# Performance work log

Hardware: AMD Instinct MI355X
Metric: run time of the kernel (lower is better)

The kernel has to match this reference:

```python
import jax, jax.numpy as jnp
import numpy as np

D_MODEL = 8      # group_channel_num = ceil(64/8)
D_INNER = 16     # expand*d_model
D_STATE = 16
D_CONV = 4
DT_RANK = 1      # ceil(d_model/16)
TOKEN_NUM = 8
GN_GROUPS = 4
EPS = 1e-5


def setup_inputs() -> dict:
    key = jax.random.key(0)
    ks = jax.random.split(key, 12)
    b, c, h, w = 4, 64, 128, 128
    s = 0.1
    return {
        "x": jax.random.normal(ks[0], (b, c, h, w), jnp.float32),
        "W_in": jax.random.normal(ks[1], (2 * D_INNER, D_MODEL), jnp.float32) * s,
        "w_conv": jax.random.normal(ks[2], (D_INNER, D_CONV), jnp.float32) * s,
        "b_conv": jax.random.normal(ks[3], (D_INNER,), jnp.float32) * s,
        "W_xproj": jax.random.normal(ks[4], (DT_RANK + 2 * D_STATE, D_INNER), jnp.float32) * s,
        "W_dt": jax.random.normal(ks[5], (D_INNER, DT_RANK), jnp.float32) * s,
        "b_dt": jax.random.normal(ks[6], (D_INNER,), jnp.float32) * s,
        "A_log": jnp.log(jnp.tile(jnp.arange(1, D_STATE + 1, dtype=jnp.float32), (D_INNER, 1))),
        "D": jnp.ones((D_INNER,), jnp.float32),
        "W_out": jax.random.normal(ks[7], (D_MODEL, D_INNER), jnp.float32) * s,
        "gamma": jnp.ones((c,), jnp.float32),
        "beta": jnp.zeros((c,), jnp.float32),
    }


def _mamba(xf, W_in, w_conv, b_conv, W_xproj, W_dt, b_dt, A_log, D, W_out):
    # xf: (N, L, d_model)
    N, L, _ = xf.shape
    xz = jnp.einsum("nld,ed->nle", xf, W_in)            # (N, L, 2*d_inner)
    xm, z = jnp.split(xz, 2, axis=-1)
    # depthwise causal conv1d, kernel d_conv, truncated to L
    xp = jnp.pad(xm, ((0, 0), (D_CONV - 1, 0), (0, 0)))
    xc = b_conv + sum(xp[:, k:k + L, :] * w_conv[:, k] for k in range(D_CONV))
    xc = jax.nn.silu(xc)                                  # (N, L, d_inner)
    dbl = jnp.einsum("nli,ei->nle", xc, W_xproj)
    dt = dbl[..., :DT_RANK]
    B = dbl[..., DT_RANK:DT_RANK + D_STATE]               # (N, L, d_state)
    C = dbl[..., DT_RANK + D_STATE:]                      # (N, L, d_state)
    delta = jax.nn.softplus(jnp.einsum("nlr,ir->nli", dt, W_dt) + b_dt)
    A = -jnp.exp(A_log)                                   # (d_inner, d_state)
    dA = jnp.exp(delta[..., None] * A)                    # (N, L, d_inner, d_state)
    dBu = delta[..., None] * B[:, :, None, :] * xc[..., None]

    def step(hst, inp):
        dA_t, dBu_t, C_t = inp
        hst = dA_t * hst + dBu_t                          # (N, d_inner, d_state)
        y_t = jnp.einsum("nis,ns->ni", hst, C_t)
        return hst, y_t

    h0 = jnp.zeros((N, D_INNER, D_STATE), xf.dtype)
    _, ys = jax.lax.scan(step, h0, (jnp.swapaxes(dA, 0, 1),
                                    jnp.swapaxes(dBu, 0, 1),
                                    jnp.swapaxes(C, 0, 1)))
    y = jnp.swapaxes(ys, 0, 1)                            # (N, L, d_inner)
    y = y + D * xc
    y = y * jax.nn.silu(z)
    return jnp.einsum("nli,oi->nlo", y, W_out)


def reference(x, W_in, w_conv, b_conv, W_xproj, W_dt, b_dt, A_log, D, W_out, gamma, beta):
    b, c, h, w = x.shape  # c == channel_num == 64, no padding needed
    xt = jnp.transpose(x, (0, 2, 3, 1)).reshape(b * h * w, TOKEN_NUM, D_MODEL)
    y = _mamba(xt, W_in, w_conv, b_conv, W_xproj, W_dt, b_dt, A_log, D, W_out)
    y = y.reshape(b, h, w, c)
    y = jnp.transpose(y, (0, 3, 1, 2))                    # (b, c, h, w)
    # GroupNorm(groups=4) + SiLU
    yr = y.reshape(b, GN_GROUPS, c // GN_GROUPS, h, w)
    mu = yr.mean(axis=(2, 3, 4), keepdims=True)
    var = yr.var(axis=(2, 3, 4), keepdims=True)
    yn = ((yr - mu) * jax.lax.rsqrt(var + EPS)).reshape(b, c, h, w)
    yn = yn * gamma[:, None, None] + beta[:, None, None]
    return x + jax.nn.silu(yn)
```

## Files before the change

kernel.cpp:

```cpp
#include <hip/hip_runtime.h>
#include <math.h>

#define BATCH 4
#define CCH 64
#define HW 16384
#define LL 8
#define DI 16
#define NSEQ (BATCH*HW)
#define CNT_PER_GROUP (16*HW)

__device__ __forceinline__ float siluf(float v) {
    return v * __builtin_amdgcn_rcpf(1.f + __expf(-v));
}

__global__ __launch_bounds__(256, 4) void mamba_kernel(
    const float* __restrict__ x, const float* __restrict__ W_in,
    const float* __restrict__ w_conv, const float* __restrict__ b_conv,
    const float* __restrict__ W_xproj, const float* __restrict__ W_dt,
    const float* __restrict__ b_dt, const float* __restrict__ Dp,
    const float* __restrict__ W_out,
    float* __restrict__ y_out,
    float* __restrict__ stats)
{
    __shared__ float xf_lds[16][68];
    __shared__ float xcy_lds[LL][16][20];
    __shared__ unsigned int proj_lds[LL][16][18];
    __shared__ float wx_lds[33][20];
    __shared__ float wout_lds[8][20];
    __shared__ float wsum_lds[4][8];

    const int t = threadIdx.x;
    const int n0 = blockIdx.x * 16;
    const int b = n0 / HW;
    const int p0 = n0 % HW;

    for (int j = t; j < 33 * 16; j += 256) wx_lds[j >> 4][j & 15] = W_xproj[j];
    for (int j = t; j < 8 * 16; j += 256) wout_lds[j >> 4][j & 15] = W_out[j];

    {
        const int wofs = t & 15;
        const int cbase = t >> 4;
        const float* xb = x + (size_t)b * CCH * HW + p0 + wofs;
#pragma unroll
        for (int it = 0; it < 4; ++it) {
            int c = cbase + 16 * it;
            xf_lds[wofs][c] = xb[(size_t)c * HW];
        }
    }

    const int s = t >> 4;
    const int i = t & 15;

    const float4 wm0 = *(const float4*)&W_in[i * 8];
    const float4 wm1 = *(const float4*)&W_in[i * 8 + 4];
    const float4 wz0 = *(const float4*)&W_in[(16 + i) * 8];
    const float4 wz1 = *(const float4*)&W_in[(16 + i) * 8 + 4];
    const float4 wcv = *(const float4*)&w_conv[i * 4];
    const float bc  = b_conv[i];
    const float wdt = W_dt[i];
    const float bdt = b_dt[i];
    const float Di  = Dp[i];

    __syncthreads();

    float xm[LL], zz[LL], xcv[LL];
#pragma unroll
    for (int l = 0; l < LL; ++l) {
        float4 xa = *(const float4*)&xf_lds[s][l * 8];
        float4 xb4 = *(const float4*)&xf_lds[s][l * 8 + 4];
        xm[l] = xa.x * wm0.x + xa.y * wm0.y + xa.z * wm0.z + xa.w * wm0.w
              + xb4.x * wm1.x + xb4.y * wm1.y + xb4.z * wm1.z + xb4.w * wm1.w;
        zz[l] = xa.x * wz0.x + xa.y * wz0.y + xa.z * wz0.z + xa.w * wz0.w
              + xb4.x * wz1.x + xb4.y * wz1.y + xb4.z * wz1.z + xb4.w * wz1.w;
    }
#pragma unroll
    for (int l = 0; l < LL; ++l) {
        float acc = bc + wcv.w * xm[l];
        if (l >= 1) acc += wcv.z * xm[l - 1];
        if (l >= 2) acc += wcv.y * xm[l - 2];
        if (l >= 3) acc += wcv.x * xm[l - 3];
        float sv = siluf(acc);
        xcv[l] = sv;
        xcy_lds[l][s][i] = sv;
    }

    float4 w0q[4], wBq[4], wCq[4];
#pragma unroll
    for (int k = 0; k < 4; ++k) {
        w0q[k] = *(const float4*)&wx_lds[0][k * 4];
        wBq[k] = *(const float4*)&wx_lds[1 + i][k * 4];
        wCq[k] = *(const float4*)&wx_lds[17 + i][k * 4];
    }
    __syncthreads();

    float dtv[LL];
#pragma unroll
    for (int l = 0; l < LL; ++l) {
        float aB = 0.f, aC = 0.f, a0 = 0.f;
#pragma unroll
        for (int k = 0; k < 4; ++k) {
            float4 xc = *(const float4*)&xcy_lds[l][s][k * 4];
            aB += xc.x * wBq[k].x + xc.y * wBq[k].y + xc.z * wBq[k].z + xc.w * wBq[k].w;
            aC += xc.x * wCq[k].x + xc.y * wCq[k].y + xc.z * wCq[k].z + xc.w * wCq[k].w;
            a0 += xc.x * w0q[k].x + xc.y * w0q[k].y + xc.z * w0q[k].z + xc.w * w0q[k].w;
        }
        unsigned int ub = (__float_as_uint(aB) + 0x8000u) >> 16;
        unsigned int uc = (__float_as_uint(aC) + 0x8000u) & 0xFFFF0000u;
        proj_lds[l][s][i] = ub | uc;
        dtv[l] = a0;
    }
    __syncthreads();

    float hst[16];
#pragma unroll
    for (int q = 0; q < 16; ++q) hst[q] = 0.f;
#pragma unroll
    for (int l = 0; l < LL; ++l) {
        float pre = dtv[l] * wdt + bdt;
        float e = __expf(pre);
        float r = __builtin_amdgcn_rcpf(1.f + e);
        float delta = (pre > 15.f) ? pre : -__logf(r);
        float u = xcv[l];
        float du = delta * u;

        unsigned int pk[16];
#pragma unroll
        for (int k = 0; k < 4; ++k)
            *(uint4*)&pk[k * 4] = *(const uint4*)&proj_lds[l][s][k * 4];

        float pw = 1.f, yl = 0.f;
#pragma unroll
        for (int q = 0; q < 16; ++q) {
            float Bv = __uint_as_float(pk[q] << 16);
            float Cv = __uint_as_float(pk[q] & 0xFFFF0000u);
            pw *= r;
            hst[q] = pw * hst[q] + du * Bv;
            yl += hst[q] * Cv;
        }
        yl += Di * u;
        yl *= siluf(zz[l]);
        xcy_lds[l][s][i] = yl;
    }
    __syncthreads();

    const int s4 = t & 15;
    const int c4 = t >> 4;
    float gsum[4], gsq[4];
#pragma unroll
    for (int it = 0; it < 4; ++it) {
        int c = c4 + 16 * it;
        int l = c >> 3, o = c & 7;
        float acc = 0.f;
#pragma unroll
        for (int k = 0; k < 4; ++k) {
            float4 yv = *(const float4*)&xcy_lds[l][s4][k * 4];
            float4 wo = *(const float4*)&wout_lds[o][k * 4];
            acc += yv.x * wo.x + yv.y * wo.y + yv.z * wo.z + yv.w * wo.w;
        }
        y_out[((size_t)b * CCH + c) * HW + p0 + s4] = acc;
        gsum[it] = acc; gsq[it] = acc * acc;
    }
#pragma unroll
    for (int ofs = 32; ofs > 0; ofs >>= 1) {
#pragma unroll
        for (int it = 0; it < 4; ++it) {
            gsum[it] += __shfl_down(gsum[it], ofs, 64);
            gsq[it]  += __shfl_down(gsq[it], ofs, 64);
        }
    }
    const int wave = t >> 6;
    if ((t & 63) == 0) {
#pragma unroll
        for (int it = 0; it < 4; ++it) {
            wsum_lds[wave][it * 2]     = gsum[it];
            wsum_lds[wave][it * 2 + 1] = gsq[it];
        }
    }
    __syncthreads();
    if (t < 8) {
        float v = wsum_lds[0][t] + wsum_lds[1][t] + wsum_lds[2][t] + wsum_lds[3][t];
        int g = t >> 1, which = t & 1;
        atomicAdd(&stats[(b * 4 + g) * 2 + which], v);
    }
}

__global__ __launch_bounds__(256) void gn_kernel(
    const float* __restrict__ x, const float* __restrict__ gamma,
    const float* __restrict__ beta, const float* __restrict__ stats,
    float* __restrict__ y)
{
    const float invcnt = 1.f / (float)CNT_PER_GROUP;
    const size_t total4 = (size_t)BATCH * CCH * HW / 4;
    for (size_t idx4 = (size_t)blockIdx.x * blockDim.x + threadIdx.x; idx4 < total4;
         idx4 += (size_t)gridDim.x * blockDim.x) {
        size_t idx = idx4 * 4;
        int bc = (int)(idx >> 14);
        int bb = bc >> 6, c = bc & 63, g = c >> 4;
        float sum = stats[(bb * 4 + g) * 2];
        float sq  = stats[(bb * 4 + g) * 2 + 1];
        float mean = sum * invcnt;
        float var  = sq * invcnt - mean * mean;
        float rstd = rsqrtf(var + 1e-5f);
        float a  = rstd * gamma[c];
        float b2 = beta[c] - mean * a;
        float4 yv = ((const float4*)y)[idx4];
        float4 xv = ((const float4*)x)[idx4];
        float4 ov;
        ov.x = xv.x + siluf(yv.x * a + b2);
        ov.y = xv.y + siluf(yv.y * a + b2);
        ov.z = xv.z + siluf(yv.z * a + b2);
        ov.w = xv.w + siluf(yv.w * a + b2);
        ((float4*)y)[idx4] = ov;
    }
}

extern "C" void kernel_launch(void* const* d_in, const int* in_sizes, int n_in,
                              void* d_out, int out_size, void* d_ws, size_t ws_size,
                              hipStream_t stream) {
    const float* x       = (const float*)d_in[0];
    const float* W_in    = (const float*)d_in[1];
    const float* w_conv  = (const float*)d_in[2];
    const float* b_conv  = (const float*)d_in[3];
    const float* W_xproj = (const float*)d_in[4];
    const float* W_dt    = (const float*)d_in[5];
    const float* b_dt    = (const float*)d_in[6];
    const float* Dp      = (const float*)d_in[8];
    const float* W_out   = (const float*)d_in[9];
    const float* gamma   = (const float*)d_in[10];
    const float* beta    = (const float*)d_in[11];
    float* out   = (float*)d_out;
    float* stats = (float*)d_ws;

    hipMemsetAsync(stats, 0, 32 * sizeof(float), stream);
    mamba_kernel<<<NSEQ / 16, 256, 0, stream>>>(
        x, W_in, w_conv, b_conv, W_xproj, W_dt, b_dt, Dp, W_out, out, stats);
    gn_kernel<<<2048, 256, 0, stream>>>(x, gamma, beta, stats, out);
}
```

Baseline: 153.3 us.

## Use packed fp16 scan, per-block partial stats, and per-batch GN coefficients

The selective-scan inner loop now keeps state and B/C in packed half2 and processes two state entries per instruction, splitting the powers of r into r..r8 and r9..r16 lanes. Global atomics on 32 stat slots are replaced by per-block partial sums written to workspace, which also removes the memset. Each GroupNorm block then reduces 1024 partials for its batch and precomputes per-channel scale and shift in shared memory. The aim is to cut scan ALU work and atomic contention, at the cost of fp16 precision for the recurrent state and redundant partial reductions in every GN block.

```diff
diff --git a/kernel.cpp b/kernel.cpp
--- a/kernel.cpp
+++ b/kernel.cpp
@@ -1,11 +1,11 @@
 #include <hip/hip_runtime.h>
+#include <hip/hip_fp16.h>
 #include <math.h>
 
 #define BATCH 4
 #define CCH 64
 #define HW 16384
 #define LL 8
-#define DI 16
 #define NSEQ (BATCH*HW)
 #define CNT_PER_GROUP (16*HW)
 
@@ -20,17 +20,18 @@
     const float* __restrict__ b_dt, const float* __restrict__ Dp,
     const float* __restrict__ W_out,
     float* __restrict__ y_out,
-    float* __restrict__ stats)
+    float* __restrict__ part)
 {
     __shared__ float xf_lds[16][68];
     __shared__ float xcy_lds[LL][16][20];
-    __shared__ unsigned int proj_lds[LL][16][18];
+    __shared__ unsigned int pj_lds[LL][16][20];
     __shared__ float wx_lds[33][20];
     __shared__ float wout_lds[8][20];
     __shared__ float wsum_lds[4][8];
 
     const int t = threadIdx.x;
-    const int n0 = blockIdx.x * 16;
+    const int blk = blockIdx.x;
+    const int n0 = blk * 16;
     const int b = n0 / HW;
     const int p0 = n0 % HW;
 
@@ -104,16 +105,15 @@
             aC += xc.x * wCq[k].x + xc.y * wCq[k].y + xc.z * wCq[k].z + xc.w * wCq[k].w;
             a0 += xc.x * w0q[k].x + xc.y * w0q[k].y + xc.z * w0q[k].z + xc.w * w0q[k].w;
         }
-        unsigned int ub = (__float_as_uint(aB) + 0x8000u) >> 16;
-        unsigned int uc = (__float_as_uint(aC) + 0x8000u) & 0xFFFF0000u;
-        proj_lds[l][s][i] = ub | uc;
+        ((unsigned short*)&pj_lds[l][s][i & 7])[i >> 3] = __half_as_ushort(__float2half(aB));
+        ((unsigned short*)&pj_lds[l][s][8 + (i & 7)])[i >> 3] = __half_as_ushort(__float2half(aC));
         dtv[l] = a0;
     }
     __syncthreads();
 
-    float hst[16];
-#pragma unroll
-    for (int q = 0; q < 16; ++q) hst[q] = 0.f;
+    __half2 h2[8];
+#pragma unroll
+    for (int j = 0; j < 8; ++j) h2[j] = __float2half2_rn(0.f);
 #pragma unroll
     for (int l = 0; l < LL; ++l) {
         float pre = dtv[l] * wdt + bdt;
@@ -122,22 +122,27 @@
         float delta = (pre > 15.f) ? pre : -__logf(r);
         float u = xcv[l];
         float du = delta * u;
-
-        unsigned int pk[16];
-#pragma unroll
-        for (int k = 0; k < 4; ++k)
-            *(uint4*)&pk[k * 4] = *(const uint4*)&proj_lds[l][s][k * 4];
-
-        float pw = 1.f, yl = 0.f;
-#pragma unroll
-        for (int q = 0; q < 16; ++q) {
-            float Bv = __uint_as_float(pk[q] << 16);
-            float Cv = __uint_as_float(pk[q] & 0xFFFF0000u);
-            pw *= r;
-            hst[q] = pw * hst[q] + du * Bv;
-            yl += hst[q] * Cv;
-        }
-        yl += Di * u;
+        float r2 = r * r, r4 = r2 * r2, r8 = r4 * r4, r9 = r8 * r;
+
+        unsigned int bw[8], cw[8];
+        *(uint4*)&bw[0] = *(const uint4*)&pj_lds[l][s][0];
+        *(uint4*)&bw[4] = *(const uint4*)&pj_lds[l][s][4];
+        *(uint4*)&cw[0] = *(const uint4*)&pj_lds[l][s][8];
+        *(uint4*)&cw[4] = *(const uint4*)&pj_lds[l][s][12];
+
+        __half2 pw2 = __floats2half2_rn(r, r9);
+        __half2 rr2 = __floats2half2_rn(r, r);
+        __half2 du2 = __floats2half2_rn(du, du);
+        __half2 y2  = __float2half2_rn(0.f);
+#pragma unroll
+        for (int j = 0; j < 8; ++j) {
+            __half2 B2 = *(__half2*)&bw[j];
+            __half2 C2 = *(__half2*)&cw[j];
+            h2[j] = __hfma2(pw2, h2[j], __hmul2(du2, B2));
+            y2 = __hfma2(h2[j], C2, y2);
+            pw2 = __hmul2(pw2, rr2);
+        }
+        float yl = __low2float(y2) + __high2float(y2) + Di * u;
         yl *= siluf(zz[l]);
         xcy_lds[l][s][i] = yl;
     }
@@ -179,30 +184,52 @@
     __syncthreads();
     if (t < 8) {
         float v = wsum_lds[0][t] + wsum_lds[1][t] + wsum_lds[2][t] + wsum_lds[3][t];
-        int g = t >> 1, which = t & 1;
-        atomicAdd(&stats[(b * 4 + g) * 2 + which], v);
+        part[(((size_t)b * 8 + t) << 10) + (blk & 1023)] = v;
     }
 }
 
 __global__ __launch_bounds__(256) void gn_kernel(
     const float* __restrict__ x, const float* __restrict__ gamma,
-    const float* __restrict__ beta, const float* __restrict__ stats,
+    const float* __restrict__ beta, const float* __restrict__ part,
     float* __restrict__ y)
 {
-    const float invcnt = 1.f / (float)CNT_PER_GROUP;
-    const size_t total4 = (size_t)BATCH * CCH * HW / 4;
-    for (size_t idx4 = (size_t)blockIdx.x * blockDim.x + threadIdx.x; idx4 < total4;
-         idx4 += (size_t)gridDim.x * blockDim.x) {
-        size_t idx = idx4 * 4;
-        int bc = (int)(idx >> 14);
-        int bb = bc >> 6, c = bc & 63, g = c >> 4;
-        float sum = stats[(bb * 4 + g) * 2];
-        float sq  = stats[(bb * 4 + g) * 2 + 1];
-        float mean = sum * invcnt;
-        float var  = sq * invcnt - mean * mean;
+    __shared__ float red_lds[8];
+    __shared__ float coef_lds[64][2];
+
+    const int t = threadIdx.x;
+    const int bb = blockIdx.x >> 9;
+    const int binb = blockIdx.x & 511;
+
+    {
+        const float* pb = part + ((size_t)bb << 13);
+        int q = t >> 5, w = t & 31;
+        float acc = 0.f;
+#pragma unroll
+        for (int k = 0; k < 32; ++k) acc += pb[(q << 10) + (k << 5) + w];
+#pragma unroll
+        for (int ofs = 16; ofs > 0; ofs >>= 1) acc += __shfl_down(acc, ofs, 32);
+        if (w == 0) red_lds[q] = acc;
+    }
+    __syncthreads();
+    if (t < 64) {
+        const float invcnt = 1.f / (float)CNT_PER_GROUP;
+        int g = t >> 4;
+        float mean = red_lds[g * 2] * invcnt;
+        float var  = red_lds[g * 2 + 1] * invcnt - mean * mean;
         float rstd = rsqrtf(var + 1e-5f);
-        float a  = rstd * gamma[c];
-        float b2 = beta[c] - mean * a;
+        float a = rstd * gamma[t];
+        coef_lds[t][0] = a;
+        coef_lds[t][1] = beta[t] - mean * a;
+    }
+    __syncthreads();
+
+#pragma unroll
+    for (int it = 0; it < 2; ++it) {
+        size_t j = (size_t)binb * 256 + t + (size_t)it * 131072;
+        int c = (int)(j >> 12);
+        float a  = coef_lds[c][0];
+        float b2 = coef_lds[c][1];
+        size_t idx4 = ((size_t)bb << 18) + j;
         float4 yv = ((const float4*)y)[idx4];
         float4 xv = ((const float4*)x)[idx4];
         float4 ov;
@@ -228,11 +255,10 @@
     const float* W_out   = (const float*)d_in[9];
     const float* gamma   = (const float*)d_in[10];
     const float* beta    = (const float*)d_in[11];
-    float* out   = (float*)d_out;
-    float* stats = (float*)d_ws;
-
-    hipMemsetAsync(stats, 0, 32 * sizeof(float), stream);
+    float* out  = (float*)d_out;
+    float* part = (float*)d_ws;
+
     mamba_kernel<<<NSEQ / 16, 256, 0, stream>>>(
-        x, W_in, w_conv, b_conv, W_xproj, W_dt, b_dt, Dp, W_out, out, stats);
-    gn_kernel<<<2048, 256, 0, stream>>>(x, gamma, beta, stats, out);
-}
+        x, W_in, w_conv, b_conv, W_xproj, W_dt, b_dt, Dp, W_out, out, part);
+    gn_kernel<<<2048, 256, 0, stream>>>(x, gamma, beta, part, out);
+}
```

Result: faster. 140.9 us (-8.1%).
